# Kernel tuning notes

Hardware: AMD Instinct MI355X
Metric: run time of the kernel (lower is better)

## Reference

```python
import jax, jax.numpy as jnp
import numpy as np
import math

B, T, C = 4, 2048, 1024
H = 16
D = C // H

def setup_inputs() -> dict:
    key = jax.random.key(0)
    k1, k2, k3 = jax.random.split(key, 3)
    x = jax.random.normal(k1, (B, T, C), dtype=jnp.float32)
    w_attn = jax.random.normal(k2, (3 * C, C), dtype=jnp.float32) * (1.0 / math.sqrt(C))
    b_attn = jnp.zeros((3 * C,), dtype=jnp.float32)
    w_proj = jax.random.normal(k3, (C, C), dtype=jnp.float32) * (1.0 / math.sqrt(C))
    b_proj = jnp.zeros((C,), dtype=jnp.float32)
    return {"x": x, "w_attn": w_attn, "b_attn": b_attn, "w_proj": w_proj, "b_proj": b_proj}

def reference(x, w_attn, b_attn, w_proj, b_proj):
    Bq, Tq, Cq = x.shape
    qkv = x @ w_attn.T + b_attn                      # [B,T,3C]
    q, k, v = jnp.split(qkv, 3, axis=-1)
    q = q.reshape(Bq, Tq, H, D).transpose(0, 2, 1, 3)  # [B,H,T,D]
    k = k.reshape(Bq, Tq, H, D).transpose(0, 2, 1, 3)
    v = v.reshape(Bq, Tq, H, D).transpose(0, 2, 1, 3)
    att = jnp.einsum('bhqd,bhkd->bhqk', q, k) * (1.0 / math.sqrt(D))
    causal = jnp.tril(jnp.ones((Tq, Tq), dtype=bool))
    att = jnp.where(causal[None, None], att, -jnp.inf)
    att = jax.nn.softmax(att, axis=-1)
    y = jnp.einsum('bhqk,bhkd->bhqd', att, v)          # [B,H,T,D]
    y = y.transpose(0, 2, 1, 3).reshape(Bq, Tq, Cq)
    return y @ w_proj.T + b_proj
```

## Files before the change

kernel.cpp:

```cpp
#include <hip/hip_runtime.h>
#include <hip/hip_bf16.h>


typedef __hip_bfloat16 bf16;
typedef __attribute__((ext_vector_type(8))) short bf16x8;
typedef __attribute__((ext_vector_type(4))) float f32x4;
typedef __attribute__((ext_vector_type(16))) float f32x16;

#define MFMA16(a, b, c) __builtin_amdgcn_mfma_f32_16x16x32_bf16(a, b, c, 0, 0, 0)
#define MFMA32(a, b, c) __builtin_amdgcn_mfma_f32_32x32x16_bf16(a, b, c, 0, 0, 0)
#define GLOAD_LDS(g, l) __builtin_amdgcn_global_load_lds( \
    (const __attribute__((address_space(1))) void*)(g),    \
    (__attribute__((address_space(3))) void*)(l), 16, 0, 0)

constexpr int Bn = 4, Tn = 2048, Cn = 1024, Hn = 16, Dn = 64;
constexpr size_t HT_ELEMS = (size_t)64 * Tn * Dn;
constexpr float QSCALE = 0.18033688011112042f;

__device__ __forceinline__ short f2bf(float f) {
    unsigned u = __float_as_uint(f);
    return (short)((u + 0x7FFF + ((u >> 16) & 1)) >> 16);
}
__device__ __forceinline__ bf16 bfbits(short s) { bf16 b; __builtin_memcpy(&b, &s, 2); return b; }

__device__ __forceinline__ unsigned cvtpk_bf16(float lo, float hi) {
    unsigned r;
    asm("v_cvt_pk_bf16_f32 %0, %1, %2" : "=v"(r) : "v"(lo), "v"(hi));
    return r;
}
__device__ __forceinline__ void permswap(unsigned& a, unsigned& b) {
#if __has_builtin(__builtin_amdgcn_permlane32_swap)
    auto r = __builtin_amdgcn_permlane32_swap(a, b, false, false);
    a = (unsigned)r[0]; b = (unsigned)r[1];
#else
    asm("v_permlane32_swap_b32 %0, %1" : "+v"(a), "+v"(b));
#endif
}
__device__ __forceinline__ bf16x8 pack4(unsigned w0, unsigned w1, unsigned w2, unsigned w3) {
    union { unsigned u[4]; bf16x8 v; } t;
    t.u[0] = w0; t.u[1] = w1; t.u[2] = w2; t.u[3] = w3;
    return t.v;
}

__global__ __launch_bounds__(256) void cast3_kernel(
    const float* __restrict__ x, const float* __restrict__ wa,
    const float* __restrict__ wp, bf16* __restrict__ out)
{
    size_t i = (size_t)blockIdx.x * 256 + threadIdx.x;
    const float* src; size_t off;
    if (i < 1048576)      { src = x;  off = i; }
    else if (i < 1441792) { src = wa; off = i - 1048576; }
    else                  { src = wp; off = i - 1441792; }
    const float4* p = (const float4*)(src + off * 8);
    float4 a = p[0], b = p[1];
    bf16x8 r;
    r[0] = f2bf(a.x); r[1] = f2bf(a.y); r[2] = f2bf(a.z); r[3] = f2bf(a.w);
    r[4] = f2bf(b.x); r[5] = f2bf(b.y); r[6] = f2bf(b.z); r[7] = f2bf(b.w);
    *(bf16x8*)(out + i * 8) = r;
}

__global__ __launch_bounds__(256) void qkv_gemm128(
    const bf16* __restrict__ Am, const bf16* __restrict__ Wm,
    const float* __restrict__ bias,
    bf16* __restrict__ qo, bf16* __restrict__ ko, bf16* __restrict__ vo)
{
    constexpr int K = 1024;
    __shared__ bf16 As[4096], Bs[4096];
    const int tid = threadIdx.x;
    const int lane = tid & 63, w = tid >> 6;
    const int row = lane & 15, quad = lane >> 4;
    const unsigned bid = blockIdx.x;
    const int x8 = bid & 7, l = bid >> 3;
    const int tm = (x8 >> 1) * 16 + l / 12;
    const int tn = (x8 & 1) * 12 + l % 12;
    const int m0 = tm * 128, n0 = tn * 128;

    const int srow = tid >> 2, skch = tid & 3;
    const bf16* ag0 = Am + (size_t)(m0 + srow) * K + skch * 8;
    const bf16* ag1 = ag0 + (size_t)64 * K;
    const bf16* wg0 = Wm + (size_t)(n0 + srow) * K + skch * 8;
    const bf16* wg1 = wg0 + (size_t)64 * K;
    bf16* asl0 = As + tid * 8;  bf16* asl1 = As + 2048 + tid * 8;
    bf16* bsl0 = Bs + tid * 8;  bf16* bsl1 = Bs + 2048 + tid * 8;

    f32x4 acc[4][4];
    #pragma unroll
    for (int i = 0; i < 4; i++)
        #pragma unroll
        for (int j = 0; j < 4; j++) acc[i][j] = {0, 0, 0, 0};

    const int r0 = (w >> 1) * 64, c0 = (w & 1) * 64;

    for (int k0 = 0; k0 < K; k0 += 32) {
        __syncthreads();
        GLOAD_LDS(ag0 + k0, asl0);
        GLOAD_LDS(ag1 + k0, asl1);
        GLOAD_LDS(wg0 + k0, bsl0);
        GLOAD_LDS(wg1 + k0, bsl1);
        __syncthreads();
        bf16x8 af[4], bfv[4];
        #pragma unroll
        for (int it = 0; it < 4; it++)
            af[it] = *(const bf16x8*)(As + (r0 + it * 16 + row) * 32 + quad * 8);
        #pragma unroll
        for (int jt = 0; jt < 4; jt++)
            bfv[jt] = *(const bf16x8*)(Bs + (c0 + jt * 16 + row) * 32 + quad * 8);
        #pragma unroll
        for (int it = 0; it < 4; it++)
            #pragma unroll
            for (int jt = 0; jt < 4; jt++)
                acc[it][jt] = MFMA16(af[it], bfv[jt], acc[it][jt]);
    }

    #pragma unroll
    for (int it = 0; it < 4; it++)
    #pragma unroll
    for (int jt = 0; jt < 4; jt++)
    #pragma unroll
    for (int r = 0; r < 4; r++) {
        int m = m0 + r0 + it * 16 + quad * 4 + r;
        int n = n0 + c0 + jt * 16 + row;
        float val = acc[it][jt][r] + bias[n];
        int which = n >> 10, cc = n & 1023;
        if (which == 0) val *= QSCALE;
        bf16 bv = bfbits(f2bf(val));
        int h = cc >> 6, d = cc & 63;
        int b = m >> 11, t = m & 2047;
        int bh = b * Hn + h;
        if (which == 0)      qo[((size_t)bh * Tn + t) * Dn + d] = bv;
        else if (which == 1) ko[((size_t)bh * Tn + t) * Dn + d] = bv;
        else                 vo[((size_t)bh * 64 + (t >> 5)) * 2048 + (size_t)d * 32 + (t & 31)] = bv;
    }
}

__global__ __launch_bounds__(256, 2) void attn_kernel(
    const bf16* __restrict__ qbp, const bf16* __restrict__ kbp,
    const bf16* __restrict__ vtb, bf16* __restrict__ ob)
{
    __shared__ __align__(128) bf16 SB[4][4096];
    __shared__ float lbufw[4][32];
    const int tid  = threadIdx.x;
    const int lane = tid & 63;
    const int w    = tid >> 6;
    const int l31  = lane & 31, hl = lane >> 5;
    const int bid  = blockIdx.x;
    const int qid  = bid & 7;
    const int idx  = bid >> 3;
    const int bh   = qid * 8 + (idx & 7);
    const int pair = idx >> 3;

    const int s2off = w * 2048 + (lane >> 3) * 128
                    + (((lane & 7) ^ ((lane >> 3) & 7)) << 4);
    const int kxor = (l31 & 7) << 4;
    const int sxor = ((l31 >> 1) & 7) << 4;

    const bf16* Q  = qbp + (size_t)bh * Tn * Dn;
    const char* Kh = (const char*)(kbp + (size_t)bh * Tn * Dn);
    const char* Vh = (const char*)vtb + (size_t)bh * 262144;

    #pragma unroll 1
    for (int sub = 0; sub < 2; sub++) {
        const int qb8   = sub ? (15 - pair) : pair;
        const int jmax2 = qb8 * 2 + 1;
        const int qtw   = qb8 * 4 + w;
        const int q0w   = qtw * 32;
        const int jd    = qtw >> 1;
        const int par   = qtw & 1;

        bf16x8 bQ[4];
        {
            const bf16* qp = Q + (size_t)(q0w + l31) * Dn + hl * 8;
            #pragma unroll
            for (int kf = 0; kf < 4; kf++) bQ[kf] = *(const bf16x8*)(qp + kf * 16);
        }

        f32x16 o2[2];
        o2[0] = {0,0,0,0,0,0,0,0,0,0,0,0,0,0,0,0};
        o2[1] = {0,0,0,0,0,0,0,0,0,0,0,0,0,0,0,0};
        float lsum = 0.f;

        GLOAD_LDS(Kh + s2off,        (char*)SB[0] + w * 2048);
        GLOAD_LDS(Kh + s2off + 1024, (char*)SB[0] + w * 2048 + 1024);
        GLOAD_LDS(Vh + s2off,        (char*)SB[2] + w * 2048);
        GLOAD_LDS(Vh + s2off + 1024, (char*)SB[2] + w * 2048 + 1024);
        __syncthreads();

        for (int j = 0; j <= jmax2; j++) {
            const int cur = j & 1;
            if (j < jmax2) {
                const int nb = cur ^ 1;
                const size_t go = (size_t)(j + 1) * 8192;
                GLOAD_LDS(Kh + go + s2off,        (char*)SB[nb] + w * 2048);
                GLOAD_LDS(Kh + go + s2off + 1024, (char*)SB[nb] + w * 2048 + 1024);
                GLOAD_LDS(Vh + go + s2off,        (char*)SB[2 + nb] + w * 2048);
                GLOAD_LDS(Vh + go + s2off + 1024, (char*)SB[2 + nb] + w * 2048 + 1024);
            }
            if (j <= jd) {
                const char* KB = (const char*)SB[cur];
                const char* VB = (const char*)SB[2 + cur];
                const bool doB = (j < jd) || par;

                bf16x8 aKa[4], aKb[4];
                #pragma unroll
                for (int kf = 0; kf < 4; kf++) {
                    const int co = ((kf * 2 + hl) << 4) ^ kxor;
                    aKa[kf] = *(const bf16x8*)(KB + l31 * 128 + co);
                    aKb[kf] = *(const bf16x8*)(KB + 4096 + l31 * 128 + co);
                }

                f32x16 sA = {0,0,0,0,0,0,0,0,0,0,0,0,0,0,0,0};
                f32x16 sB = {0,0,0,0,0,0,0,0,0,0,0,0,0,0,0,0};
                __builtin_amdgcn_s_setprio(1);
                #pragma unroll
                for (int kf = 0; kf < 4; kf++) sA = MFMA32(aKa[kf], bQ[kf], sA);
                if (doB) {
                    #pragma unroll
                    for (int kf = 0; kf < 4; kf++) sB = MFMA32(aKb[kf], bQ[kf], sB);
                }
                __builtin_amdgcn_s_setprio(0);

                bf16x8 vfL[4], vfH[4];
                #pragma unroll
                for (int i2 = 0; i2 < 4; i2++) {
                    const int vh = i2 >> 1, kc = i2 & 1;
                    const int off = (vh * 16 + (l31 >> 1)) * 128
                                  + ((((l31 & 1) * 4 + kc * 2 + hl) << 4) ^ sxor);
                    vfL[i2] = *(const bf16x8*)(VB + off);
                    if (doB) vfH[i2] = *(const bf16x8*)(VB + 4096 + off);
                }

                float pA[16];
                if (j == jd && par == 0) {
                    #pragma unroll
                    for (int r = 0; r < 16; r++) {
                        const int krow = (r & 3) + 8 * (r >> 2) + 4 * hl;
                        float e = exp2f(sA[r]);
                        pA[r] = (krow > l31) ? 0.f : e;
                    }
                } else {
                    #pragma unroll
                    for (int r = 0; r < 16; r++) pA[r] = exp2f(sA[r]);
                }
                lsum += (((pA[0]+pA[1]) + (pA[2]+pA[3])) + ((pA[4]+pA[5]) + (pA[6]+pA[7])))
                      + (((pA[8]+pA[9]) + (pA[10]+pA[11])) + ((pA[12]+pA[13]) + (pA[14]+pA[15])));

                unsigned a0 = cvtpk_bf16(pA[0],  pA[1]),  b0 = cvtpk_bf16(pA[4],  pA[5]);
                unsigned a1 = cvtpk_bf16(pA[2],  pA[3]),  b1 = cvtpk_bf16(pA[6],  pA[7]);
                unsigned a2 = cvtpk_bf16(pA[8],  pA[9]),  b2 = cvtpk_bf16(pA[12], pA[13]);
                unsigned a3 = cvtpk_bf16(pA[10], pA[11]), b3 = cvtpk_bf16(pA[14], pA[15]);
                permswap(a0, b0); permswap(a1, b1); permswap(a2, b2); permswap(a3, b3);
                const bf16x8 PA0 = pack4(a0, a1, b0, b1);
                const bf16x8 PA1 = pack4(a2, a3, b2, b3);

                __builtin_amdgcn_s_setprio(1);
                o2[0] = MFMA32(PA0, vfL[0], o2[0]);
                o2[0] = MFMA32(PA1, vfL[1], o2[0]);
                o2[1] = MFMA32(PA0, vfL[2], o2[1]);
                o2[1] = MFMA32(PA1, vfL[3], o2[1]);
                __builtin_amdgcn_s_setprio(0);

                if (doB) {
                    float pB[16];
                    if (j == jd) {
                        #pragma unroll
                        for (int r = 0; r < 16; r++) {
                            const int krow = (r & 3) + 8 * (r >> 2) + 4 * hl;
                            float e = exp2f(sB[r]);
                            pB[r] = (krow > l31) ? 0.f : e;
                        }
                    } else {
                        #pragma unroll
                        for (int r = 0; r < 16; r++) pB[r] = exp2f(sB[r]);
                    }
                    lsum += (((pB[0]+pB[1]) + (pB[2]+pB[3])) + ((pB[4]+pB[5]) + (pB[6]+pB[7])))
                          + (((pB[8]+pB[9]) + (pB[10]+pB[11])) + ((pB[12]+pB[13]) + (pB[14]+pB[15])));

                    unsigned c0_ = cvtpk_bf16(pB[0],  pB[1]),  d0_ = cvtpk_bf16(pB[4],  pB[5]);
                    unsigned c1_ = cvtpk_bf16(pB[2],  pB[3]),  d1_ = cvtpk_bf16(pB[6],  pB[7]);
                    unsigned c2_ = cvtpk_bf16(pB[8],  pB[9]),  d2_ = cvtpk_bf16(pB[12], pB[13]);
                    unsigned c3_ = cvtpk_bf16(pB[10], pB[11]), d3_ = cvtpk_bf16(pB[14], pB[15]);
                    permswap(c0_, d0_); permswap(c1_, d1_); permswap(c2_, d2_); permswap(c3_, d3_);
                    const bf16x8 PB0 = pack4(c0_, c1_, d0_, d1_);
                    const bf16x8 PB1 = pack4(c2_, c3_, d2_, d3_);

                    __builtin_amdgcn_s_setprio(1);
                    o2[0] = MFMA32(PB0, vfH[0], o2[0]);
                    o2[0] = MFMA32(PB1, vfH[1], o2[0]);
                    o2[1] = MFMA32(PB0, vfH[2], o2[1]);
                    o2[1] = MFMA32(PB1, vfH[3], o2[1]);
                    __builtin_amdgcn_s_setprio(0);
                }
            }
            __syncthreads();
        }

        unsigned lsu = __float_as_uint(lsum), lsv = lsu;
        permswap(lsu, lsv);
        const float ltot = __uint_as_float(lsu) + __uint_as_float(lsv);
        if (hl == 0) lbufw[w][l31] = 1.0f / ltot;
        asm volatile("s_waitcnt lgkmcnt(0)" ::: "memory");

        char* obl = (char*)SB[w];
        #pragma unroll
        for (int r = 0; r < 16; r++) {
            const int q  = (r & 3) + 8 * (r >> 2) + 4 * hl;
            const float rl = lbufw[w][q];
            const int qx = (q & 7) << 4;
            *(short*)(obl + q * 128 + ((2 * l31) ^ qx))      = f2bf(o2[0][r] * rl);
            *(short*)(obl + q * 128 + ((64 + 2 * l31) ^ qx)) = f2bf(o2[1][r] * rl);
        }
        asm volatile("s_waitcnt lgkmcnt(0)" ::: "memory");

        {
            const int q = lane >> 1, half = lane & 1;
            const int qx = (q & 7) << 4;
            const int b = bh >> 4, h = bh & 15;
            bf16* gdst = ob + ((size_t)(b * Tn + (q0w + q))) * Cn + h * Dn + half * 32;
            #pragma unroll
            for (int c = 0; c < 4; c++) {
                bf16x8 rv = *(const bf16x8*)(obl + q * 128 + (((half * 64) + c * 16) ^ qx));
                *(bf16x8*)(gdst + c * 8) = rv;
            }
        }
        __syncthreads();
    }
}

__global__ __launch_bounds__(256) void proj_gemm128(
    const bf16* __restrict__ Am, const bf16* __restrict__ Wm,
    const float* __restrict__ bias, float* __restrict__ out)
{
    constexpr int K = 1024;
    __shared__ bf16 As[4096], Bs[4096];
    const int tid = threadIdx.x;
    const int lane = tid & 63, w = tid >> 6;
    const int row = lane & 15, quad = lane >> 4;
    const unsigned bid = blockIdx.x;
    const int x8 = bid & 7, l = bid >> 3;
    const int tm = x8 * 8 + l / 8;
    const int tn = l % 8;
    const int m0 = tm * 128, n0 = tn * 128;

    const int srow = tid >> 2, skch = tid & 3;
    const bf16* ag0 = Am + (size_t)(m0 + srow) * K + skch * 8;
    const bf16* ag1 = ag0 + (size_t)64 * K;
    const bf16* wg0 = Wm + (size_t)(n0 + srow) * K + skch * 8;
    const bf16* wg1 = wg0 + (size_t)64 * K;
    bf16* asl0 = As + tid * 8;  bf16* asl1 = As + 2048 + tid * 8;
    bf16* bsl0 = Bs + tid * 8;  bf16* bsl1 = Bs + 2048 + tid * 8;

    f32x4 acc[4][4];
    #pragma unroll
    for (int i = 0; i < 4; i++)
        #pragma unroll
        for (int j = 0; j < 4; j++) acc[i][j] = {0, 0, 0, 0};

    const int r0 = (w >> 1) * 64, c0 = (w & 1) * 64;

    for (int k0 = 0; k0 < K; k0 += 32) {
        __syncthreads();
        GLOAD_LDS(ag0 + k0, asl0);
        GLOAD_LDS(ag1 + k0, asl1);
        GLOAD_LDS(wg0 + k0, bsl0);
        GLOAD_LDS(wg1 + k0, bsl1);
        __syncthreads();
        bf16x8 af[4], bfv[4];
        #pragma unroll
        for (int it = 0; it < 4; it++)
            af[it] = *(const bf16x8*)(As + (r0 + it * 16 + row) * 32 + quad * 8);
        #pragma unroll
        for (int jt = 0; jt < 4; jt++)
            bfv[jt] = *(const bf16x8*)(Bs + (c0 + jt * 16 + row) * 32 + quad * 8);
        #pragma unroll
        for (int it = 0; it < 4; it++)
            #pragma unroll
            for (int jt = 0; jt < 4; jt++)
                acc[it][jt] = MFMA16(af[it], bfv[jt], acc[it][jt]);
    }

    #pragma unroll
    for (int it = 0; it < 4; it++)
    #pragma unroll
    for (int jt = 0; jt < 4; jt++)
    #pragma unroll
    for (int r = 0; r < 4; r++) {
        int m = m0 + r0 + it * 16 + quad * 4 + r;
        int n = n0 + c0 + jt * 16 + row;
        out[(size_t)m * 1024 + n] = acc[it][jt][r] + bias[n];
    }
}

extern "C" void kernel_launch(void* const* d_in, const int* in_sizes, int n_in,
                              void* d_out, int out_size, void* d_ws, size_t ws_size,
                              hipStream_t stream) {
    const float* x      = (const float*)d_in[0];
    const float* w_attn = (const float*)d_in[1];
    const float* b_attn = (const float*)d_in[2];
    const float* w_proj = (const float*)d_in[3];
    const float* b_proj = (const float*)d_in[4];
    float* out = (float*)d_out;

    bf16* ws  = (bf16*)((char*)d_ws + 1024);
    bf16* xb  = ws;
    bf16* wab = xb  + (size_t)8192 * 1024;
    bf16* wpb = wab + (size_t)3072 * 1024;
    bf16* q   = wpb + (size_t)1024 * 1024;
    bf16* k   = q  + HT_ELEMS;
    bf16* vt  = k  + HT_ELEMS;
    bf16* o   = vt + HT_ELEMS;

    cast3_kernel<<<6144, 256, 0, stream>>>(x, w_attn, w_proj, xb);

    qkv_gemm128 <<<64 * 24, 256, 0, stream>>>(xb, wab, b_attn, q, k, vt);
    attn_kernel <<<512, 256, 0, stream>>>(q, k, vt, o);
    proj_gemm128<<<64 * 8, 256, 0, stream>>>(o, wpb, b_proj, out);
}
```

Baseline: 289.1 us.

## Double-buffer LDS tiles in QKV and projection GEMMs to overlap loads with MFMA

Both GEMM kernels now use two LDS buffers per operand. The next K-slice is issued via global_load_lds while MFMAs run on the current slice, coordinated with explicit vmcnt/lgkmcnt waits and raw s_barriers. This targets the load-then-compute serialization of the single-buffer loop. In exchange it doubles shared memory per block, which may reduce occupancy, and correctness now depends on hand-placed waitcnt counts.

```diff
diff --git a/kernel.cpp b/kernel.cpp
--- a/kernel.cpp
+++ b/kernel.cpp
@@ -65,7 +65,7 @@
     bf16* __restrict__ qo, bf16* __restrict__ ko, bf16* __restrict__ vo)
 {
     constexpr int K = 1024;
-    __shared__ bf16 As[4096], Bs[4096];
+    __shared__ bf16 As[2][4096], Bs[2][4096];
     const int tid = threadIdx.x;
     const int lane = tid & 63, w = tid >> 6;
     const int row = lane & 15, quad = lane >> 4;
@@ -80,8 +80,6 @@
     const bf16* ag1 = ag0 + (size_t)64 * K;
     const bf16* wg0 = Wm + (size_t)(n0 + srow) * K + skch * 8;
     const bf16* wg1 = wg0 + (size_t)64 * K;
-    bf16* asl0 = As + tid * 8;  bf16* asl1 = As + 2048 + tid * 8;
-    bf16* bsl0 = Bs + tid * 8;  bf16* bsl1 = Bs + 2048 + tid * 8;
 
     f32x4 acc[4][4];
     #pragma unroll
@@ -91,26 +89,51 @@
 
     const int r0 = (w >> 1) * 64, c0 = (w & 1) * 64;
 
-    for (int k0 = 0; k0 < K; k0 += 32) {
-        __syncthreads();
-        GLOAD_LDS(ag0 + k0, asl0);
-        GLOAD_LDS(ag1 + k0, asl1);
-        GLOAD_LDS(wg0 + k0, bsl0);
-        GLOAD_LDS(wg1 + k0, bsl1);
-        __syncthreads();
-        bf16x8 af[4], bfv[4];
-        #pragma unroll
-        for (int it = 0; it < 4; it++)
-            af[it] = *(const bf16x8*)(As + (r0 + it * 16 + row) * 32 + quad * 8);
-        #pragma unroll
-        for (int jt = 0; jt < 4; jt++)
-            bfv[jt] = *(const bf16x8*)(Bs + (c0 + jt * 16 + row) * 32 + quad * 8);
-        #pragma unroll
-        for (int it = 0; it < 4; it++)
-            #pragma unroll
-            for (int jt = 0; jt < 4; jt++)
-                acc[it][jt] = MFMA16(af[it], bfv[jt], acc[it][jt]);
+#define G_STAGE(b, ko) do {                               \
+        GLOAD_LDS(ag0 + (ko), &As[b][tid * 8]);           \
+        GLOAD_LDS(ag1 + (ko), &As[b][2048 + tid * 8]);    \
+        GLOAD_LDS(wg0 + (ko), &Bs[b][tid * 8]);           \
+        GLOAD_LDS(wg1 + (ko), &Bs[b][2048 + tid * 8]);    \
+    } while (0)
+
+#define G_COMPUTE(b) do {                                                      \
+        bf16x8 af[4], bfv[4];                                                  \
+        _Pragma("unroll")                                                      \
+        for (int it = 0; it < 4; it++)                                         \
+            af[it] = *(const bf16x8*)(&As[b][(r0 + it * 16 + row) * 32 + quad * 8]); \
+        _Pragma("unroll")                                                      \
+        for (int jt = 0; jt < 4; jt++)                                         \
+            bfv[jt] = *(const bf16x8*)(&Bs[b][(c0 + jt * 16 + row) * 32 + quad * 8]); \
+        _Pragma("unroll")                                                      \
+        for (int it = 0; it < 4; it++)                                         \
+            _Pragma("unroll")                                                  \
+            for (int jt = 0; jt < 4; jt++)                                     \
+                acc[it][jt] = MFMA16(af[it], bfv[jt], acc[it][jt]);            \
+    } while (0)
+
+    G_STAGE(0, 0);
+    for (int k0 = 0; k0 < K; k0 += 64) {
+        G_STAGE(1, k0 + 32);
+        asm volatile("s_waitcnt vmcnt(4)" ::: "memory");
+        __builtin_amdgcn_s_barrier();
+        G_COMPUTE(0);
+        asm volatile("s_waitcnt lgkmcnt(0)" ::: "memory");
+        __builtin_amdgcn_sched_barrier(0);
+        __builtin_amdgcn_s_barrier();
+        if (k0 + 64 < K) {
+            G_STAGE(0, k0 + 64);
+            asm volatile("s_waitcnt vmcnt(4)" ::: "memory");
+        } else {
+            asm volatile("s_waitcnt vmcnt(0)" ::: "memory");
+        }
+        __builtin_amdgcn_s_barrier();
+        G_COMPUTE(1);
+        asm volatile("s_waitcnt lgkmcnt(0)" ::: "memory");
+        __builtin_amdgcn_sched_barrier(0);
+        __builtin_amdgcn_s_barrier();
     }
+#undef G_STAGE
+#undef G_COMPUTE
 
     #pragma unroll
     for (int it = 0; it < 4; it++)
@@ -331,7 +354,7 @@
     const float* __restrict__ bias, float* __restrict__ out)
 {
     constexpr int K = 1024;
-    __shared__ bf16 As[4096], Bs[4096];
+    __shared__ bf16 As[2][4096], Bs[2][4096];
     const int tid = threadIdx.x;
     const int lane = tid & 63, w = tid >> 6;
     const int row = lane & 15, quad = lane >> 4;
@@ -346,8 +369,6 @@
     const bf16* ag1 = ag0 + (size_t)64 * K;
     const bf16* wg0 = Wm + (size_t)(n0 + srow) * K + skch * 8;
     const bf16* wg1 = wg0 + (size_t)64 * K;
-    bf16* asl0 = As + tid * 8;  bf16* asl1 = As + 2048 + tid * 8;
-    bf16* bsl0 = Bs + tid * 8;  bf16* bsl1 = Bs + 2048 + tid * 8;
 
     f32x4 acc[4][4];
     #pragma unroll
@@ -357,26 +378,51 @@
 
     const int r0 = (w >> 1) * 64, c0 = (w & 1) * 64;
 
-    for (int k0 = 0; k0 < K; k0 += 32) {
-        __syncthreads();
-        GLOAD_LDS(ag0 + k0, asl0);
-        GLOAD_LDS(ag1 + k0, asl1);
-        GLOAD_LDS(wg0 + k0, bsl0);
-        GLOAD_LDS(wg1 + k0, bsl1);
-        __syncthreads();
-        bf16x8 af[4], bfv[4];
-        #pragma unroll
-        for (int it = 0; it < 4; it++)
-            af[it] = *(const bf16x8*)(As + (r0 + it * 16 + row) * 32 + quad * 8);
-        #pragma unroll
-        for (int jt = 0; jt < 4; jt++)
-            bfv[jt] = *(const bf16x8*)(Bs + (c0 + jt * 16 + row) * 32 + quad * 8);
-        #pragma unroll
-        for (int it = 0; it < 4; it++)
-            #pragma unroll
-            for (int jt = 0; jt < 4; jt++)
-                acc[it][jt] = MFMA16(af[it], bfv[jt], acc[it][jt]);
+#define G_STAGE(b, ko) do {                               \
+        GLOAD_LDS(ag0 + (ko), &As[b][tid * 8]);           \
+        GLOAD_LDS(ag1 + (ko), &As[b][2048 + tid * 8]);    \
+        GLOAD_LDS(wg0 + (ko), &Bs[b][tid * 8]);           \
+        GLOAD_LDS(wg1 + (ko), &Bs[b][2048 + tid * 8]);    \
+    } while (0)
+
+#define G_COMPUTE(b) do {                                                      \
+        bf16x8 af[4], bfv[4];                                                  \
+        _Pragma("unroll")                                                      \
+        for (int it = 0; it < 4; it++)                                         \
+            af[it] = *(const bf16x8*)(&As[b][(r0 + it * 16 + row) * 32 + quad * 8]); \
+        _Pragma("unroll")                                                      \
+        for (int jt = 0; jt < 4; jt++)                                         \
+            bfv[jt] = *(const bf16x8*)(&Bs[b][(c0 + jt * 16 + row) * 32 + quad * 8]); \
+        _Pragma("unroll")                                                      \
+        for (int it = 0; it < 4; it++)                                         \
+            _Pragma("unroll")                                                  \
+            for (int jt = 0; jt < 4; jt++)                                     \
+                acc[it][jt] = MFMA16(af[it], bfv[jt], acc[it][jt]);            \
+    } while (0)
+
+    G_STAGE(0, 0);
+    for (int k0 = 0; k0 < K; k0 += 64) {
+        G_STAGE(1, k0 + 32);
+        asm volatile("s_waitcnt vmcnt(4)" ::: "memory");
+        __builtin_amdgcn_s_barrier();
+        G_COMPUTE(0);
+        asm volatile("s_waitcnt lgkmcnt(0)" ::: "memory");
+        __builtin_amdgcn_sched_barrier(0);
+        __builtin_amdgcn_s_barrier();
+        if (k0 + 64 < K) {
+            G_STAGE(0, k0 + 64);
+            asm volatile("s_waitcnt vmcnt(4)" ::: "memory");
+        } else {
+            asm volatile("s_waitcnt vmcnt(0)" ::: "memory");
+        }
+        __builtin_amdgcn_s_barrier();
+        G_COMPUTE(1);
+        asm volatile("s_waitcnt lgkmcnt(0)" ::: "memory");
+        __builtin_amdgcn_sched_barrier(0);
+        __builtin_amdgcn_s_barrier();
     }
+#undef G_STAGE
+#undef G_COMPUTE
 
     #pragma unroll
     for (int it = 0; it < 4; it++)
```

After: 297.3 us. 1.03x slower.

## Rewrite QKV GEMM with 256x192 tiles, double-buffered swizzled LDS, 8 waves

Applied to the files above, without the earlier changes.

Replaces the 128x128 single-buffered QKV GEMM with a 256x192-tile kernel using 512 threads, a K-step of 64, double-buffered LDS, and XOR-swizzled LDS layout to avoid bank conflicts. Global-to-LDS loads for the next stage are issued while MFMAs for the current stage run, with explicit barriers and priority hints. Larger tiles raise arithmetic intensity and cut redundant global reads, at the cost of a single block per CU and heavy LDS use (about 112KB).

```diff
diff --git a/kernel.cpp b/kernel.cpp
--- a/kernel.cpp
+++ b/kernel.cpp
@@ -59,68 +59,129 @@
     *(bf16x8*)(out + i * 8) = r;
 }
 
-__global__ __launch_bounds__(256) void qkv_gemm128(
+__global__ __launch_bounds__(512, 1) void qkv_gemm256(
     const bf16* __restrict__ Am, const bf16* __restrict__ Wm,
     const float* __restrict__ bias,
     bf16* __restrict__ qo, bf16* __restrict__ ko, bf16* __restrict__ vo)
 {
     constexpr int K = 1024;
-    __shared__ bf16 As[4096], Bs[4096];
-    const int tid = threadIdx.x;
-    const int lane = tid & 63, w = tid >> 6;
-    const int row = lane & 15, quad = lane >> 4;
+    __shared__ __align__(128) bf16 As[2][16384];
+    __shared__ __align__(128) bf16 Bs[2][12288];
+    const int tid  = threadIdx.x;
+    const int lane = tid & 63;
+    const int wid  = tid >> 6, wm = wid >> 2, wn = wid & 3;
+    const int row16 = lane & 15, quad = lane >> 4;
     const unsigned bid = blockIdx.x;
     const int x8 = bid & 7, l = bid >> 3;
-    const int tm = (x8 >> 1) * 16 + l / 12;
-    const int tn = (x8 & 1) * 12 + l % 12;
-    const int m0 = tm * 128, n0 = tn * 128;
-
-    const int srow = tid >> 2, skch = tid & 3;
-    const bf16* ag0 = Am + (size_t)(m0 + srow) * K + skch * 8;
-    const bf16* ag1 = ag0 + (size_t)64 * K;
-    const bf16* wg0 = Wm + (size_t)(n0 + srow) * K + skch * 8;
-    const bf16* wg1 = wg0 + (size_t)64 * K;
-    bf16* asl0 = As + tid * 8;  bf16* asl1 = As + 2048 + tid * 8;
-    bf16* bsl0 = Bs + tid * 8;  bf16* bsl1 = Bs + 2048 + tid * 8;
-
-    f32x4 acc[4][4];
-    #pragma unroll
-    for (int i = 0; i < 4; i++)
-        #pragma unroll
-        for (int j = 0; j < 4; j++) acc[i][j] = {0, 0, 0, 0};
-
-    const int r0 = (w >> 1) * 64, c0 = (w & 1) * 64;
-
-    for (int k0 = 0; k0 < K; k0 += 32) {
-        __syncthreads();
-        GLOAD_LDS(ag0 + k0, asl0);
-        GLOAD_LDS(ag1 + k0, asl1);
-        GLOAD_LDS(wg0 + k0, bsl0);
-        GLOAD_LDS(wg1 + k0, bsl1);
-        __syncthreads();
-        bf16x8 af[4], bfv[4];
-        #pragma unroll
-        for (int it = 0; it < 4; it++)
-            af[it] = *(const bf16x8*)(As + (r0 + it * 16 + row) * 32 + quad * 8);
-        #pragma unroll
-        for (int jt = 0; jt < 4; jt++)
-            bfv[jt] = *(const bf16x8*)(Bs + (c0 + jt * 16 + row) * 32 + quad * 8);
-        #pragma unroll
-        for (int it = 0; it < 4; it++)
-            #pragma unroll
-            for (int jt = 0; jt < 4; jt++)
-                acc[it][jt] = MFMA16(af[it], bfv[jt], acc[it][jt]);
+    const int tm = (x8 >> 1) * 8 + l / 8;
+    const int tn = (x8 & 1) * 8 + l % 8;
+    const int m0 = tm * 256, n0 = tn * 192;
+
+    const int rL = tid >> 3;
+    const int cS = (tid & 7) ^ (rL & 7);
+    const char* Ab = (const char*)Am;
+    const char* Bb = (const char*)Wm;
+
+    const int axor = (row16 & 7) << 4;
+
+    f32x4 acc[8][3];
+    #pragma unroll
+    for (int i = 0; i < 8; i++)
+        #pragma unroll
+        for (int j = 0; j < 3; j++) acc[i][j] = {0, 0, 0, 0};
+
+#define STAGE_A(nb, k0) do {                                                    \
+        _Pragma("unroll")                                                       \
+        for (int g = 0; g < 4; g++)                                             \
+            GLOAD_LDS(Ab + (size_t)(m0 + g * 64 + rL) * 2048 + (k0) * 2 + cS * 16, \
+                      (char*)As[nb] + g * 8192 + tid * 16);                     \
+    } while (0)
+#define STAGE_B(nb, k0) do {                                                    \
+        _Pragma("unroll")                                                       \
+        for (int g = 0; g < 3; g++)                                             \
+            GLOAD_LDS(Bb + (size_t)(n0 + g * 64 + rL) * 2048 + (k0) * 2 + cS * 16, \
+                      (char*)Bs[nb] + g * 8192 + tid * 16);                     \
+    } while (0)
+#define DS_A(MQ, KK) do {                                                       \
+        _Pragma("unroll")                                                       \
+        for (int f = 0; f < 4; f++)                                             \
+            aR[f] = *(const bf16x8*)(Ac + (wm * 128 + (MQ) * 64 + f * 16 + row16) * 128 \
+                                        + (((KK) * 64 + quad * 16) ^ axor));    \
+    } while (0)
+#define DS_B(KK) do {                                                           \
+        _Pragma("unroll")                                                       \
+        for (int f = 0; f < 3; f++)                                             \
+            bR[f] = *(const bf16x8*)(Bc + (wn * 48 + f * 16 + row16) * 128      \
+                                        + (((KK) * 64 + quad * 16) ^ axor));    \
+    } while (0)
+#define MF12(MQ) do {                                                           \
+        _Pragma("unroll")                                                       \
+        for (int mf4 = 0; mf4 < 4; mf4++)                                       \
+            _Pragma("unroll")                                                   \
+            for (int nf = 0; nf < 3; nf++)                                      \
+                acc[(MQ) * 4 + mf4][nf] = MFMA16(aR[mf4], bR[nf], acc[(MQ) * 4 + mf4][nf]); \
+    } while (0)
+
+    STAGE_A(0, 0);
+    STAGE_B(0, 0);
+    asm volatile("s_waitcnt vmcnt(0)" ::: "memory");
+    __syncthreads();
+
+    for (int t = 0; t < 16; ++t) {
+        const int cur = t & 1, nxt = cur ^ 1;
+        const char* Ac = (const char*)As[cur];
+        const char* Bc = (const char*)Bs[cur];
+        const int k1 = (t + 1) * 64;
+        bf16x8 aR[4], bR[3];
+
+        if (t < 15) STAGE_A(nxt, k1);
+        DS_A(0, 0);
+        DS_B(0);
+        __builtin_amdgcn_s_barrier();
+        asm volatile("s_waitcnt lgkmcnt(0)" ::: "memory");
+        __builtin_amdgcn_sched_barrier(0);
+        __builtin_amdgcn_s_setprio(1);  MF12(0);  __builtin_amdgcn_s_setprio(0);
+        __builtin_amdgcn_s_barrier();
+
+        if (t < 15) STAGE_B(nxt, k1);
+        DS_A(1, 0);
+        __builtin_amdgcn_s_barrier();
+        asm volatile("s_waitcnt lgkmcnt(0)" ::: "memory");
+        __builtin_amdgcn_sched_barrier(0);
+        __builtin_amdgcn_s_setprio(1);  MF12(1);  __builtin_amdgcn_s_setprio(0);
+        __builtin_amdgcn_s_barrier();
+
+        DS_A(0, 1);
+        DS_B(1);
+        __builtin_amdgcn_s_barrier();
+        asm volatile("s_waitcnt lgkmcnt(0)" ::: "memory");
+        __builtin_amdgcn_sched_barrier(0);
+        __builtin_amdgcn_s_setprio(1);  MF12(0);  __builtin_amdgcn_s_setprio(0);
+        __builtin_amdgcn_s_barrier();
+
+        DS_A(1, 1);
+        __builtin_amdgcn_s_barrier();
+        asm volatile("s_waitcnt lgkmcnt(0)" ::: "memory");
+        __builtin_amdgcn_sched_barrier(0);
+        __builtin_amdgcn_s_setprio(1);  MF12(1);  __builtin_amdgcn_s_setprio(0);
+        asm volatile("s_waitcnt vmcnt(0)" ::: "memory");
+        __builtin_amdgcn_s_barrier();
     }
-
-    #pragma unroll
-    for (int it = 0; it < 4; it++)
-    #pragma unroll
-    for (int jt = 0; jt < 4; jt++)
+#undef STAGE_A
+#undef STAGE_B
+#undef DS_A
+#undef DS_B
+#undef MF12
+
+    #pragma unroll
+    for (int mf = 0; mf < 8; mf++)
+    #pragma unroll
+    for (int nf = 0; nf < 3; nf++)
     #pragma unroll
     for (int r = 0; r < 4; r++) {
-        int m = m0 + r0 + it * 16 + quad * 4 + r;
-        int n = n0 + c0 + jt * 16 + row;
-        float val = acc[it][jt][r] + bias[n];
+        int m = m0 + wm * 128 + mf * 16 + quad * 4 + r;
+        int n = n0 + wn * 48 + nf * 16 + row16;
+        float val = acc[mf][nf][r] + bias[n];
         int which = n >> 10, cc = n & 1023;
         if (which == 0) val *= QSCALE;
         bf16 bv = bfbits(f2bf(val));
@@ -411,7 +472,7 @@
 
     cast3_kernel<<<6144, 256, 0, stream>>>(x, w_attn, w_proj, xb);
 
-    qkv_gemm128 <<<64 * 24, 256, 0, stream>>>(xb, wab, b_attn, q, k, vt);
+    qkv_gemm256 <<<512, 512, 0, stream>>>(xb, wab, b_attn, q, k, vt);
     attn_kernel <<<512, 256, 0, stream>>>(q, k, vt, o);
     proj_gemm128<<<64 * 8, 256, 0, stream>>>(o, wpb, b_proj, out);
 }
```

Result: slower. 294.9 us (+2.0%).
